# Performance work log

Measured on AMD Instinct MI355X. Metric: run time of the kernel, lower is better.

The kernel has to match this reference:

```python
import jax, jax.numpy as jnp
import numpy as np

B, C, H, W = 8, 8, 512, 512

# one-pixel shifts with zero padding (equivalent to the bmm with shift matrices)
def shift_right(x):  # out[..., c] = x[..., c-1]
    return jnp.pad(x, ((0, 0), (0, 0), (1, 0)))[:, :, :-1]
def shift_left(x):   # out[..., c] = x[..., c+1]
    return jnp.pad(x, ((0, 0), (0, 0), (0, 1)))[:, :, 1:]
def shift_up(x):     # out[r] = x[r+1]
    return jnp.pad(x, ((0, 0), (0, 1), (0, 0)))[:, 1:, :]
def shift_down(x):   # out[r] = x[r-1]
    return jnp.pad(x, ((0, 0), (1, 0), (0, 0)))[:, :-1, :]

def bilater_voting(c):
    # c: [B, 8, H, W] probabilities
    right        = shift_right(c[:, 4])
    left         = shift_left(c[:, 3])
    left_bottom  = shift_left(shift_down(c[:, 5]))
    right_above  = shift_right(shift_up(c[:, 2]))
    left_above   = shift_left(shift_up(c[:, 0]))
    bottom       = shift_down(c[:, 6])
    up           = shift_up(c[:, 1])
    right_bottom = shift_right(shift_down(c[:, 7]))
    a1 = c[:, 3] * right
    a2 = c[:, 4] * left
    a3 = c[:, 1] * bottom
    a4 = c[:, 6] * up
    a5 = c[:, 2] * left_bottom
    a6 = c[:, 5] * right_above
    a7 = c[:, 0] * right_bottom
    a8 = c[:, 7] * left_above
    vote_out = jnp.stack([a7, a3, a5, a1, a2, a6, a4, a8], axis=1)
    glo_map = jnp.mean(vote_out, axis=1)
    return glo_map, vote_out

def bce(p, t):
    # matches torch F.binary_cross_entropy (mean reduction, log clamped at -100)
    logp = jnp.clip(jnp.log(p), -100.0, None)
    log1mp = jnp.clip(jnp.log(1.0 - p), -100.0, None)
    return -jnp.mean(t * logp + (1.0 - t) * log1mp)

def setup_inputs() -> dict:
    key = jax.random.key(0)
    k1, k2, k3, k4 = jax.random.split(key, 4)
    atts = jax.random.normal(k1, (B, C, H, W), dtype=jnp.float32)
    dets = jax.random.normal(k2, (B, C, H, W), dtype=jnp.float32)
    target = jax.random.randint(k3, (B, 1, H, W), 0, 2).astype(jnp.float32)
    con_target = jax.random.randint(k4, (B, C, H, W), 0, 2).astype(jnp.float32)
    return {"atts": atts, "dets": dets, "target": target, "con_target": con_target}

def reference(atts, dets, target, con_target):
    # edge mask from connectivity GT: pixels with 0 < sum < 8
    sum_conn = jnp.sum(con_target, axis=1)  # [B, H, W]
    edge_conn = jnp.where((sum_conn < 8.0) & (sum_conn > 0.0), 1.0, 0.0)

    atts_p = jax.nn.sigmoid(atts)
    dets_p = jax.nn.sigmoid(dets)

    glo_map1, vote_out1 = bilater_voting(atts_p)
    glo_map2, vote_out2 = bilater_voting(dets_p)

    # edge/decouple loss on dets branch
    pred_mask_min = 1.0 - jnp.min(vote_out2, axis=1)
    pred_mask_min = pred_mask_min * edge_conn
    decouple_map = glo_map2 * (1.0 - edge_conn) + pred_mask_min
    de_loss2 = bce(decouple_map[:, None], target)

    bce_loss1 = bce(glo_map1[:, None], target)
    bicon_loss1 = bce(vote_out1, con_target)
    conn_loss1 = bce(atts_p, con_target)
    bicon_loss2 = bce(vote_out2, con_target)
    conn_loss2 = bce(dets_p, con_target)

    loss = (0.2 * bicon_loss1 + 0.8 * conn_loss1 + bce_loss1
            + 0.2 * bicon_loss2 + 0.8 * conn_loss2 + de_loss2)
    return loss
```

## Files before the change

kernel.cpp:

```cpp
#include <hip/hip_runtime.h>

#define BB 8
#define CC 8
#define HH 512
#define WW 512
#define HWSZ (HH * WW)

typedef float v4 __attribute__((ext_vector_type(4)));

__device__ __forceinline__ v4 uload4(const float* __restrict__ p) {
    v4 r;
    __builtin_memcpy(&r, p, sizeof(v4));
    return r;
}
__device__ __forceinline__ v4 aload4(const float* __restrict__ p) {
    return *(const v4* __restrict__)p;
}

__device__ __forceinline__ v4 sig4(v4 x) {
    v4 r;
#pragma unroll
    for (int i = 0; i < 4; ++i)
        r[i] = __builtin_amdgcn_rcpf(1.0f + __expf(-x[i]));
    return r;
}

__device__ __forceinline__ float bce2(float p, float t) {
    float sel = (t > 0.5f) ? p : (1.0f - p);
    return -fmaxf(__log2f(sel), -144.26950409f);
}

__device__ __forceinline__ void branch_eval(
    const float* __restrict__ base,
    int offC, int offU, int offD,
    float mh0, float mh1, v4 mwL, v4 mwR,
    const v4* __restrict__ conv4,
    v4& glo, v4& vmin, float& bicon, float& conn)
{
    v4 s[8];
#pragma unroll
    for (int c = 0; c < 8; ++c)
        s[c] = sig4(aload4(base + c * HWSZ + offC));

    v4 n[8];
    n[0] = sig4(uload4(base + 7 * HWSZ + offU - 1)) * (mh0 * mwL);
    n[1] = sig4(aload4(base + 6 * HWSZ + offU    )) *  mh0;
    n[2] = sig4(uload4(base + 5 * HWSZ + offU + 1)) * (mh0 * mwR);
    n[3] = sig4(uload4(base + 4 * HWSZ + offC - 1)) *  mwL;
    n[4] = sig4(uload4(base + 3 * HWSZ + offC + 1)) *  mwR;
    n[5] = sig4(uload4(base + 2 * HWSZ + offD - 1)) * (mh1 * mwL);
    n[6] = sig4(aload4(base + 1 * HWSZ + offD    )) *  mh1;
    n[7] = sig4(uload4(base + 0 * HWSZ + offD + 1)) * (mh1 * mwR);

    v4 vsum = {0.0f, 0.0f, 0.0f, 0.0f};
    vmin = {1e30f, 1e30f, 1e30f, 1e30f};
    bicon = 0.0f;
    conn = 0.0f;
#pragma unroll
    for (int k = 0; k < 8; ++k) {
        v4 v = s[k] * n[k];
        vsum += v;
        vmin = __builtin_elementwise_min(vmin, v);
#pragma unroll
        for (int i = 0; i < 4; ++i) {
            bicon += bce2(v[i],    conv4[k][i]);
            conn  += bce2(s[k][i], conv4[k][i]);
        }
    }
    glo = vsum * 0.125f;
}

__global__ __launch_bounds__(256) void bicon_loss_kernel(
    const float* __restrict__ atts, const float* __restrict__ dets,
    const float* __restrict__ target, const float* __restrict__ con,
    float* __restrict__ out)
{
    const int idx = blockIdx.x * 256 + threadIdx.x;
    const int w0  = (idx & 127) << 2;
    const int row = idx >> 7;
    const int h   = row & (HH - 1);
    const int b   = row >> 9;

    const int hm = (h > 0) ? h - 1 : 0;
    const int hp = (h < HH - 1) ? h + 1 : HH - 1;
    const float mh0 = (h > 0) ? 1.0f : 0.0f;
    const float mh1 = (h < HH - 1) ? 1.0f : 0.0f;
    v4 mwL = {(w0 == 0) ? 0.0f : 1.0f, 1.0f, 1.0f, 1.0f};
    v4 mwR = {1.0f, 1.0f, 1.0f, (w0 == WW - 4) ? 0.0f : 1.0f};

    const int offC = h * WW + w0;
    const int offU = hm * WW + w0;
    const int offD = hp * WW + w0;

    const float* cbase = con + b * CC * HWSZ;
    v4 conv4[8];
    v4 csum = {0.0f, 0.0f, 0.0f, 0.0f};
#pragma unroll
    for (int c = 0; c < 8; ++c) {
        conv4[c] = aload4(cbase + c * HWSZ + offC);
        csum += conv4[c];
    }
    v4 edge;
#pragma unroll
    for (int i = 0; i < 4; ++i)
        edge[i] = (csum[i] < 8.0f && csum[i] > 0.0f) ? 1.0f : 0.0f;

    const v4 t4 = aload4(target + b * HWSZ + offC);

    v4 glo1, vmin1, glo2, vmin2;
    float bi1, co1, bi2, co2;
    branch_eval(atts + b * CC * HWSZ, offC, offU, offD, mh0, mh1, mwL, mwR,
                conv4, glo1, vmin1, bi1, co1);
    branch_eval(dets + b * CC * HWSZ, offC, offU, offD, mh0, mh1, mwL, mwR,
                conv4, glo2, vmin2, bi2, co2);

    float pix = 0.0f;
#pragma unroll
    for (int i = 0; i < 4; ++i) {
        float dec = glo2[i] * (1.0f - edge[i]) + (1.0f - vmin2[i]) * edge[i];
        pix += bce2(glo1[i], t4[i]) + bce2(dec, t4[i]);
    }

    const float wbic = 0.2f / (float)(BB * CC * HWSZ);
    const float wcon = 0.8f / (float)(BB * CC * HWSZ);
    const float wpix = 1.0f / (float)(BB * HWSZ);
    const float ln2  = 0.69314718056f;

    float local = (wbic * (bi1 + bi2) + wcon * (co1 + co2) + wpix * pix) * ln2;

#pragma unroll
    for (int off = 32; off > 0; off >>= 1)
        local += __shfl_down(local, off, 64);

    __shared__ float wsum[4];
    const int lane = threadIdx.x & 63;
    const int wid  = threadIdx.x >> 6;
    if (lane == 0) wsum[wid] = local;
    __syncthreads();
    if (threadIdx.x == 0) {
        float s = wsum[0] + wsum[1] + wsum[2] + wsum[3];
        atomicAdd(out, s);
    }
}

extern "C" void kernel_launch(void* const* d_in, const int* in_sizes, int n_in,
                              void* d_out, int out_size, void* d_ws, size_t ws_size,
                              hipStream_t stream) {
    const float* atts   = (const float*)d_in[0];
    const float* dets   = (const float*)d_in[1];
    const float* target = (const float*)d_in[2];
    const float* con    = (const float*)d_in[3];
    float* out = (float*)d_out;

    hipMemsetAsync(out, 0, sizeof(float), stream);

    const int ngroups = BB * HH * WW / 4;
    bicon_loss_kernel<<<ngroups / 256, 256, 0, stream>>>(atts, dets, target, con, out);
}
```

Before: 201.4 us.

## Fold per-channel BCE logs into products and preload all inputs

```diff
diff --git a/kernel.cpp b/kernel.cpp
--- a/kernel.cpp
+++ b/kernel.cpp
@@ -7,6 +7,8 @@
 #define HWSZ (HH * WW)
 
 typedef float v4 __attribute__((ext_vector_type(4)));
+
+#define LOG2_CLAMP -144.26950409f
 
 __device__ __forceinline__ v4 uload4(const float* __restrict__ p) {
     v4 r;
@@ -25,52 +27,51 @@
     return r;
 }
 
-__device__ __forceinline__ float bce2(float p, float t) {
-    float sel = (t > 0.5f) ? p : (1.0f - p);
-    return -fmaxf(__log2f(sel), -144.26950409f);
+__device__ __forceinline__ v4 vsel(v4 t, v4 x, v4 y) {
+    v4 r;
+#pragma unroll
+    for (int i = 0; i < 4; ++i) r[i] = (t[i] > 0.5f) ? x[i] : y[i];
+    return r;
 }
 
-__device__ __forceinline__ void branch_eval(
-    const float* __restrict__ base,
-    int offC, int offU, int offD,
-    float mh0, float mh1, v4 mwL, v4 mwR,
-    const v4* __restrict__ conv4,
-    v4& glo, v4& vmin, float& bicon, float& conn)
+template <bool NEED_MIN>
+__device__ __forceinline__ void eval_branch(
+    const v4* __restrict__ cr, const v4* __restrict__ nr,
+    const v4* __restrict__ cv, const v4* __restrict__ mk,
+    v4& glo, v4& vmin, float& Lbic, float& Lcon)
 {
-    v4 s[8];
-#pragma unroll
-    for (int c = 0; c < 8; ++c)
-        s[c] = sig4(aload4(base + c * HWSZ + offC));
+    v4 pb0 = {1.f, 1.f, 1.f, 1.f}, pb1 = {1.f, 1.f, 1.f, 1.f};
+    v4 pc  = {1.f, 1.f, 1.f, 1.f};
+    v4 vsum = {0.f, 0.f, 0.f, 0.f};
+    if (NEED_MIN) vmin = {1e30f, 1e30f, 1e30f, 1e30f};
+    v4 one = {1.f, 1.f, 1.f, 1.f};
 
-    v4 n[8];
-    n[0] = sig4(uload4(base + 7 * HWSZ + offU - 1)) * (mh0 * mwL);
-    n[1] = sig4(aload4(base + 6 * HWSZ + offU    )) *  mh0;
-    n[2] = sig4(uload4(base + 5 * HWSZ + offU + 1)) * (mh0 * mwR);
-    n[3] = sig4(uload4(base + 4 * HWSZ + offC - 1)) *  mwL;
-    n[4] = sig4(uload4(base + 3 * HWSZ + offC + 1)) *  mwR;
-    n[5] = sig4(uload4(base + 2 * HWSZ + offD - 1)) * (mh1 * mwL);
-    n[6] = sig4(aload4(base + 1 * HWSZ + offD    )) *  mh1;
-    n[7] = sig4(uload4(base + 0 * HWSZ + offD + 1)) * (mh1 * mwR);
-
-    v4 vsum = {0.0f, 0.0f, 0.0f, 0.0f};
-    vmin = {1e30f, 1e30f, 1e30f, 1e30f};
-    bicon = 0.0f;
-    conn = 0.0f;
 #pragma unroll
     for (int k = 0; k < 8; ++k) {
-        v4 v = s[k] * n[k];
+        v4 s = sig4(cr[k]);
+        v4 n = sig4(nr[k]) * mk[k];
+        v4 v = s * n;
         vsum += v;
-        vmin = __builtin_elementwise_min(vmin, v);
-#pragma unroll
-        for (int i = 0; i < 4; ++i) {
-            bicon += bce2(v[i],    conv4[k][i]);
-            conn  += bce2(s[k][i], conv4[k][i]);
-        }
+        if (NEED_MIN) vmin = __builtin_elementwise_min(vmin, v);
+        v4 t  = cv[k];
+        v4 av = vsel(t, v, one - v);
+        v4 as = vsel(t, s, one - s);
+        if (k < 4) pb0 *= av; else pb1 *= av;
+        pc *= as;
     }
     glo = vsum * 0.125f;
+
+    float lb = 0.f, lc = 0.f;
+#pragma unroll
+    for (int i = 0; i < 4; ++i) {
+        lb += fmaxf(__log2f(pb0[i]), LOG2_CLAMP) + fmaxf(__log2f(pb1[i]), LOG2_CLAMP);
+        lc += fmaxf(__log2f(pc[i]), LOG2_CLAMP);
+    }
+    Lbic = lb;
+    Lcon = lc;
 }
 
-__global__ __launch_bounds__(256) void bicon_loss_kernel(
+__global__ __launch_bounds__(256, 2) void bicon_loss_kernel(
     const float* __restrict__ atts, const float* __restrict__ dets,
     const float* __restrict__ target, const float* __restrict__ con,
     float* __restrict__ out)
@@ -85,40 +86,72 @@
     const int hp = (h < HH - 1) ? h + 1 : HH - 1;
     const float mh0 = (h > 0) ? 1.0f : 0.0f;
     const float mh1 = (h < HH - 1) ? 1.0f : 0.0f;
-    v4 mwL = {(w0 == 0) ? 0.0f : 1.0f, 1.0f, 1.0f, 1.0f};
-    v4 mwR = {1.0f, 1.0f, 1.0f, (w0 == WW - 4) ? 0.0f : 1.0f};
+    const v4 mwL = {(w0 == 0) ? 0.0f : 1.0f, 1.f, 1.f, 1.f};
+    const v4 mwR = {1.f, 1.f, 1.f, (w0 == WW - 4) ? 0.0f : 1.0f};
 
     const int offC = h * WW + w0;
     const int offU = hm * WW + w0;
     const int offD = hp * WW + w0;
 
-    const float* cbase = con + b * CC * HWSZ;
-    v4 conv4[8];
-    v4 csum = {0.0f, 0.0f, 0.0f, 0.0f};
+    const float* __restrict__ ab = atts + b * CC * HWSZ;
+    const float* __restrict__ db = dets + b * CC * HWSZ;
+    const float* __restrict__ cb = con  + b * CC * HWSZ;
+
+    v4 ac[8], an[8], dc[8], dn[8], cv[8], t4;
 #pragma unroll
-    for (int c = 0; c < 8; ++c) {
-        conv4[c] = aload4(cbase + c * HWSZ + offC);
-        csum += conv4[c];
-    }
+    for (int c = 0; c < 8; ++c) ac[c] = aload4(ab + c * HWSZ + offC);
+    an[0] = uload4(ab + 7 * HWSZ + offU - 1);
+    an[1] = aload4(ab + 6 * HWSZ + offU);
+    an[2] = uload4(ab + 5 * HWSZ + offU + 1);
+    an[3] = uload4(ab + 4 * HWSZ + offC - 1);
+    an[4] = uload4(ab + 3 * HWSZ + offC + 1);
+    an[5] = uload4(ab + 2 * HWSZ + offD - 1);
+    an[6] = aload4(ab + 1 * HWSZ + offD);
+    an[7] = uload4(ab + 0 * HWSZ + offD + 1);
+#pragma unroll
+    for (int c = 0; c < 8; ++c) dc[c] = aload4(db + c * HWSZ + offC);
+    dn[0] = uload4(db + 7 * HWSZ + offU - 1);
+    dn[1] = aload4(db + 6 * HWSZ + offU);
+    dn[2] = uload4(db + 5 * HWSZ + offU + 1);
+    dn[3] = uload4(db + 4 * HWSZ + offC - 1);
+    dn[4] = uload4(db + 3 * HWSZ + offC + 1);
+    dn[5] = uload4(db + 2 * HWSZ + offD - 1);
+    dn[6] = aload4(db + 1 * HWSZ + offD);
+    dn[7] = uload4(db + 0 * HWSZ + offD + 1);
+#pragma unroll
+    for (int c = 0; c < 8; ++c) cv[c] = aload4(cb + c * HWSZ + offC);
+    t4 = aload4(target + b * HWSZ + offC);
+
+    v4 mk[8];
+    mk[0] = mwL * mh0;
+    mk[1] = {mh0, mh0, mh0, mh0};
+    mk[2] = mwR * mh0;
+    mk[3] = mwL;
+    mk[4] = mwR;
+    mk[5] = mwL * mh1;
+    mk[6] = {mh1, mh1, mh1, mh1};
+    mk[7] = mwR * mh1;
+
+    v4 csum = {0.f, 0.f, 0.f, 0.f};
+#pragma unroll
+    for (int c = 0; c < 8; ++c) csum += cv[c];
     v4 edge;
 #pragma unroll
     for (int i = 0; i < 4; ++i)
         edge[i] = (csum[i] < 8.0f && csum[i] > 0.0f) ? 1.0f : 0.0f;
 
-    const v4 t4 = aload4(target + b * HWSZ + offC);
+    v4 glo1, glo2, vmin1, vmin2;
+    float Lb1, Lc1, Lb2, Lc2;
+    eval_branch<false>(ac, an, cv, mk, glo1, vmin1, Lb1, Lc1);
+    eval_branch<true >(dc, dn, cv, mk, glo2, vmin2, Lb2, Lc2);
 
-    v4 glo1, vmin1, glo2, vmin2;
-    float bi1, co1, bi2, co2;
-    branch_eval(atts + b * CC * HWSZ, offC, offU, offD, mh0, mh1, mwL, mwR,
-                conv4, glo1, vmin1, bi1, co1);
-    branch_eval(dets + b * CC * HWSZ, offC, offU, offD, mh0, mh1, mwL, mwR,
-                conv4, glo2, vmin2, bi2, co2);
-
-    float pix = 0.0f;
+    float Lp = 0.f;
 #pragma unroll
     for (int i = 0; i < 4; ++i) {
-        float dec = glo2[i] * (1.0f - edge[i]) + (1.0f - vmin2[i]) * edge[i];
-        pix += bce2(glo1[i], t4[i]) + bce2(dec, t4[i]);
+        float dec = (edge[i] > 0.5f) ? (1.0f - vmin2[i]) : glo2[i];
+        float a  = (t4[i] > 0.5f) ? glo1[i] : 1.0f - glo1[i];
+        float bs = (t4[i] > 0.5f) ? dec     : 1.0f - dec;
+        Lp += fmaxf(__log2f(a * bs), LOG2_CLAMP);
     }
 
     const float wbic = 0.2f / (float)(BB * CC * HWSZ);
@@ -126,7 +159,7 @@
     const float wpix = 1.0f / (float)(BB * HWSZ);
     const float ln2  = 0.69314718056f;
 
-    float local = (wbic * (bi1 + bi2) + wcon * (co1 + co2) + wpix * pix) * ln2;
+    float local = -(wbic * (Lb1 + Lb2) + wcon * (Lc1 + Lc2) + wpix * Lp) * ln2;
 
 #pragma unroll
     for (int off = 32; off > 0; off >>= 1)
```

New measurement: 200.8 us. No clear change (-0.3%).
